# Kernel optimization log

Measured on AMD Instinct MI355X. Metric: run time of the kernel, lower is better.

The kernel has to match this reference:

```python
import jax, jax.numpy as jnp
import numpy as np

HASH_BINS = 100000
EMB = 64
B = 262144


def _glorot(key, shape):
    fan_in, fan_out = shape[0], shape[-1]
    std = np.sqrt(2.0 / (fan_in + fan_out)).astype(np.float32)
    return jax.random.normal(key, shape, dtype=jnp.float32) * std


def setup_inputs() -> dict:
    key = jax.random.key(0)
    ks = jax.random.split(key, 16)
    return {
        "user_idx": jax.random.randint(ks[0], (B,), 0, HASH_BINS, dtype=jnp.int32),
        "item_idx": jax.random.randint(ks[1], (B,), 0, HASH_BINS, dtype=jnp.int32),
        "user_emb": jax.random.normal(ks[2], (HASH_BINS, EMB), dtype=jnp.float32) * 0.05,
        "item_emb": jax.random.normal(ks[3], (HASH_BINS, EMB), dtype=jnp.float32) * 0.05,
        "lin_w": jax.random.normal(ks[4], (2 * HASH_BINS,), dtype=jnp.float32) * 0.01,
        "lin_b": jnp.zeros((1,), jnp.float32),
        "cross_k": _glorot(ks[5], (2 * EMB, 2 * EMB)),
        "W1": _glorot(ks[6], (2 * EMB, 200)), "b1": jnp.zeros((200,), jnp.float32),
        "W2": _glorot(ks[7], (200, 256)),     "b2": jnp.zeros((256,), jnp.float32),
        "W3": _glorot(ks[8], (256, 200)),     "b3": jnp.zeros((200,), jnp.float32),
        "W4": _glorot(ks[9], (200, 128)),     "b4": jnp.zeros((128,), jnp.float32),
        "W5": _glorot(ks[10], (128, 1)),      "b5": jnp.zeros((1,), jnp.float32),
    }


def reference(user_idx, item_idx, user_emb, item_emb, lin_w, lin_b, cross_k,
              W1, b1, W2, b2, W3, b3, W4, b4, W5, b5):
    # Embedding lookups (flattened + concatenated): [B, 2*EMB]
    emb = jnp.concatenate([user_emb[user_idx], item_emb[item_idx]], axis=1)

    # FM linear term. CategoryEncoding(multi-hot over 2*HASH_BINS) -> Dense(1)
    # is exactly a gather-sum of the dense kernel rows (one user + one item token).
    linear = (lin_w[user_idx] + lin_w[HASH_BINS + item_idx] + lin_b)[:, None]  # [B,1]

    # FM cross term: 0.5 * mean((xK)^2 - x^2 K^2, axis=1)
    xk = emb @ cross_k                      # [B, 128]
    x2k2 = (emb * emb) @ (cross_k * cross_k)
    cross = 0.5 * jnp.mean(xk * xk - x2k2, axis=1, keepdims=True)  # [B,1]

    # Deep MLP (inference: no dropout)
    h = jax.nn.relu(emb @ W1 + b1)
    h = jax.nn.relu(h @ W2 + b2)
    h = jax.nn.relu(h @ W3 + b3)
    h = jax.nn.relu(h @ W4 + b4)
    dnn = h @ W5 + b5                       # [B,1]

    return jax.nn.sigmoid(linear + cross + dnn)
```

## Files before the change

### kernel.cpp

```cpp
#include <hip/hip_runtime.h>

#define HASH_BINS 100000
#define EMBD 64
#define BATCH 262144
#define BM 64
#define SA 264
#define SB 232

typedef __attribute__((ext_vector_type(8))) short short8;
typedef __attribute__((ext_vector_type(4))) float floatx4;
typedef __attribute__((ext_vector_type(4))) unsigned short ushortx4;

static __device__ __forceinline__ unsigned short f2bf(float f) {
  unsigned u = __builtin_bit_cast(unsigned, f);
  u += 0x7fff + ((u >> 16) & 1);
  return (unsigned short)(u >> 16);
}
static __device__ __forceinline__ float bf2f(unsigned short b) {
  return __builtin_bit_cast(float, ((unsigned)b) << 16);
}

__global__ void dfm_prep(const float* __restrict__ K, const float* __restrict__ W1,
                         const float* __restrict__ W2, const float* __restrict__ W3,
                         const float* __restrict__ W4,
                         float* __restrict__ S, unsigned short* __restrict__ Kt,
                         unsigned short* __restrict__ W1t, unsigned short* __restrict__ W2t,
                         unsigned short* __restrict__ W3t, unsigned short* __restrict__ W4t)
{
  int idx = blockIdx.x * 256 + threadIdx.x;
  if (idx < 128) {
    float s = 0.f;
    for (int j = 0; j < 128; j++) { float v = K[idx * 128 + j]; s += v * v; }
    S[idx] = s;
  }
  int i = idx;
  if (i < 16384) {
    int k = i >> 7, n = i & 127;
    Kt[n * 128 + k] = f2bf(K[i]);
  } else if ((i -= 16384) < 25600) {
    int k = i / 200, n = i - k * 200;
    W1t[n * 128 + k] = f2bf(W1[i]);
  } else if ((i -= 25600) < 3072) {
    int n = 200 + (i >> 7), k = i & 127;
    W1t[n * 128 + k] = 0;
  } else if ((i -= 3072) < 51200) {
    int k = i >> 8, n = i & 255;
    W2t[n * 224 + k] = f2bf(W2[i]);
  } else if ((i -= 51200) < 6144) {
    int n = i / 24, k = 200 + (i - n * 24);
    W2t[n * 224 + k] = 0;
  } else if ((i -= 6144) < 51200) {
    int k = i / 200, n = i - k * 200;
    W3t[n * 256 + k] = f2bf(W3[i]);
  } else if ((i -= 51200) < 6144) {
    int n = 200 + (i >> 8), k = i & 255;
    W3t[n * 256 + k] = 0;
  } else if ((i -= 6144) < 25600) {
    int k = i >> 7, n = i & 127;
    W4t[n * 224 + k] = f2bf(W4[i]);
  } else if ((i -= 25600) < 3072) {
    int n = i / 24, k = 200 + (i - n * 24);
    W4t[n * 224 + k] = 0;
  }
}

template <int KP, int CH>
static __device__ __forceinline__ void mfma_pass(const unsigned short* __restrict__ wt,
                                                 int tileRow0, const unsigned short* actIn,
                                                 int sin, int m, int qd, floatx4* acc)
{
#pragma unroll
  for (int i = 0; i < CH * 4; i++) acc[i] = {0.f, 0.f, 0.f, 0.f};
#pragma unroll
  for (int ks = 0; ks < KP / 32; ks++) {
    short8 a[4];
#pragma unroll
    for (int rt = 0; rt < 4; rt++)
      a[rt] = *(const short8*)&actIn[(rt * 16 + m) * sin + ks * 32 + qd * 8];
#pragma unroll
    for (int n = 0; n < CH; n++) {
      short8 w = *(const short8*)&wt[(tileRow0 + n * 16 + m) * KP + ks * 32 + qd * 8];
#pragma unroll
      for (int rt = 0; rt < 4; rt++)
        acc[n * 4 + rt] = __builtin_amdgcn_mfma_f32_16x16x32_bf16(w, a[rt], acc[n * 4 + rt], 0, 0, 0);
    }
  }
}

template <int CH>
static __device__ __forceinline__ void epilogue_relu(const float* __restrict__ bias,
                                                     int colBase, int nreal,
                                                     unsigned short* actOut, int sout,
                                                     int m, int qd, const floatx4* acc)
{
#pragma unroll
  for (int n = 0; n < CH; n++) {
    int col = colBase + n * 16 + qd * 4;
    float b0 = 0.f, b1 = 0.f, b2 = 0.f, b3 = 0.f;
    if (col < nreal) {
      float4 q = *(const float4*)(bias + col);
      b0 = q.x; b1 = q.y; b2 = q.z; b3 = q.w;
    }
#pragma unroll
    for (int rt = 0; rt < 4; rt++) {
      ushortx4 h = { f2bf(fmaxf(acc[n * 4 + rt][0] + b0, 0.f)),
                     f2bf(fmaxf(acc[n * 4 + rt][1] + b1, 0.f)),
                     f2bf(fmaxf(acc[n * 4 + rt][2] + b2, 0.f)),
                     f2bf(fmaxf(acc[n * 4 + rt][3] + b3, 0.f)) };
      *(ushortx4*)&actOut[(rt * 16 + m) * sout + col] = h;
    }
  }
}

__global__ __launch_bounds__(512)
void dfm_main(const int* __restrict__ uidx, const int* __restrict__ iidx,
              const float* __restrict__ uemb, const float* __restrict__ iemb,
              const float* __restrict__ linw, const float* __restrict__ linb,
              const float* __restrict__ b1, const float* __restrict__ b2,
              const float* __restrict__ b3, const float* __restrict__ b4,
              const float* __restrict__ W5, const float* __restrict__ b5,
              const float* __restrict__ S, const unsigned short* __restrict__ Wc,
              const unsigned short* __restrict__ W2t, const unsigned short* __restrict__ W3t,
              const unsigned short* __restrict__ W4t,
              float* __restrict__ out)
{
  __shared__ unsigned short actA[BM * SA];
  __shared__ unsigned short actB[BM * SB];
  __shared__ float crosspart[4][BM];
  __shared__ float part[BM][8];
  __shared__ float linrow[BM];

  const int t = threadIdx.x;
  const int lane = t & 63, wave = t >> 6;
  const int m = lane & 15, qd = lane >> 4;
  const int r = t >> 3, c = t & 7;

  {
    int g = blockIdx.x * BM + r;
    int u = uidx[g], it = iidx[g];
    const float* up = uemb + (long)u * EMBD + c * 8;
    const float* ip = iemb + (long)it * EMBD + c * 8;
    float qp = 0.f;
#pragma unroll
    for (int j = 0; j < 8; j += 4) {
      float4 f = *(const float4*)(up + j);
      int col = c * 8 + j;
      float4 sv = *(const float4*)(S + col);
      ushortx4 h = {f2bf(f.x), f2bf(f.y), f2bf(f.z), f2bf(f.w)};
      *(ushortx4*)&actA[r * SA + col] = h;
      qp += f.x * f.x * sv.x + f.y * f.y * sv.y + f.z * f.z * sv.z + f.w * f.w * sv.w;
    }
#pragma unroll
    for (int j = 0; j < 8; j += 4) {
      float4 f = *(const float4*)(ip + j);
      int col = 64 + c * 8 + j;
      float4 sv = *(const float4*)(S + col);
      ushortx4 h = {f2bf(f.x), f2bf(f.y), f2bf(f.z), f2bf(f.w)};
      *(ushortx4*)&actA[r * SA + col] = h;
      qp += f.x * f.x * sv.x + f.y * f.y * sv.y + f.z * f.z * sv.z + f.w * f.w * sv.w;
    }
    part[r][c] = qp;
    if (c == 0) linrow[r] = linw[u] + linw[HASH_BINS + it] + linb[0];
  }
  __syncthreads();

  if (wave < 4) {
    floatx4 acc[8];
    mfma_pass<128, 2>(Wc, (2 * wave) * 16, actA, SA, m, qd, acc);
    float s[4];
#pragma unroll
    for (int rt = 0; rt < 4; rt++) {
      s[rt] = 0.f;
#pragma unroll
      for (int n = 0; n < 2; n++)
#pragma unroll
        for (int i = 0; i < 4; i++)
          s[rt] += acc[n * 4 + rt][i] * acc[n * 4 + rt][i];
      s[rt] += __shfl_xor(s[rt], 16, 64);
      s[rt] += __shfl_xor(s[rt], 32, 64);
    }
    if (qd == 0)
#pragma unroll
      for (int rt = 0; rt < 4; rt++)
        crosspart[wave][rt * 16 + m] = s[rt];
    floatx4 acc2[4];
    mfma_pass<128, 1>(Wc, 128 + wave * 16, actA, SA, m, qd, acc2);
    epilogue_relu<1>(b1, wave * 16, 200, actB, SB, m, qd, acc2);
  } else if (wave < 6) {
    int s0 = 4 + (wave - 4) * 3;
    floatx4 acc[12];
    mfma_pass<128, 3>(Wc, 128 + s0 * 16, actA, SA, m, qd, acc);
    epilogue_relu<3>(b1, s0 * 16, 200, actB, SB, m, qd, acc);
  } else {
    int s0 = 10 + (wave - 6) * 2;
    floatx4 acc[8];
    mfma_pass<128, 2>(Wc, 128 + s0 * 16, actA, SA, m, qd, acc);
    epilogue_relu<2>(b1, s0 * 16, 200, actB, SB, m, qd, acc);
  }
  __syncthreads();

  {
    floatx4 acc[8];
    mfma_pass<224, 2>(W2t, wave * 2 * 16, actB, SB, m, qd, acc);
    epilogue_relu<2>(b2, wave * 2 * 16, 256, actA, SA, m, qd, acc);
  }
  __syncthreads();

  if (wave < 6) {
    floatx4 acc[8];
    mfma_pass<256, 2>(W3t, wave * 2 * 16, actA, SA, m, qd, acc);
    epilogue_relu<2>(b3, wave * 2 * 16, 200, actB, SB, m, qd, acc);
  } else {
    int s0 = 12 + (wave - 6);
    floatx4 acc[4];
    mfma_pass<256, 1>(W3t, s0 * 16, actA, SA, m, qd, acc);
    epilogue_relu<1>(b3, s0 * 16, 200, actB, SB, m, qd, acc);
  }
  __syncthreads();

  {
    floatx4 acc[4];
    mfma_pass<224, 1>(W4t, wave * 16, actB, SB, m, qd, acc);
    epilogue_relu<1>(b4, wave * 16, 128, actA, SA, m, qd, acc);
  }
  __syncthreads();

  {
    float qp = part[r][c];
    float d = 0.f;
    const unsigned short* ap = &actA[r * SA + c * 16];
#pragma unroll
    for (int j = 0; j < 2; j++) {
      short8 h = *(const short8*)(ap + j * 8);
      float4 w0 = *(const float4*)(W5 + c * 16 + j * 8);
      float4 w1 = *(const float4*)(W5 + c * 16 + j * 8 + 4);
      d += bf2f((unsigned short)h[0]) * w0.x + bf2f((unsigned short)h[1]) * w0.y +
           bf2f((unsigned short)h[2]) * w0.z + bf2f((unsigned short)h[3]) * w0.w +
           bf2f((unsigned short)h[4]) * w1.x + bf2f((unsigned short)h[5]) * w1.y +
           bf2f((unsigned short)h[6]) * w1.z + bf2f((unsigned short)h[7]) * w1.w;
    }
    const float inv = 0.5f / 128.f;
    part[r][c] = d - inv * qp;
    __syncthreads();
    if (c == 0) {
      float xk2 = crosspart[0][r] + crosspart[1][r] + crosspart[2][r] + crosspart[3][r];
      float dnn = part[r][0] + part[r][1] + part[r][2] + part[r][3] +
                  part[r][4] + part[r][5] + part[r][6] + part[r][7];
      float logit = linrow[r] + inv * xk2 + dnn + b5[0];
      out[blockIdx.x * BM + r] = 1.f / (1.f + expf(-logit));
    }
  }
}

extern "C" void kernel_launch(void* const* d_in, const int* in_sizes, int n_in,
                              void* d_out, int out_size, void* d_ws, size_t ws_size,
                              hipStream_t stream)
{
  const int*   uidx = (const int*)d_in[0];
  const int*   iidx = (const int*)d_in[1];
  const float* uemb = (const float*)d_in[2];
  const float* iemb = (const float*)d_in[3];
  const float* linw = (const float*)d_in[4];
  const float* linb = (const float*)d_in[5];
  const float* K    = (const float*)d_in[6];
  const float* W1   = (const float*)d_in[7];
  const float* b1   = (const float*)d_in[8];
  const float* W2   = (const float*)d_in[9];
  const float* b2   = (const float*)d_in[10];
  const float* W3   = (const float*)d_in[11];
  const float* b3   = (const float*)d_in[12];
  const float* W4   = (const float*)d_in[13];
  const float* b4   = (const float*)d_in[14];
  const float* W5   = (const float*)d_in[15];
  const float* b5   = (const float*)d_in[16];

  char* w = (char*)d_ws;
  float* S = (float*)w;
  unsigned short* Kt  = (unsigned short*)(w + 512);
  unsigned short* W1t = (unsigned short*)(w + 33280);
  unsigned short* W2t = (unsigned short*)(w + 90624);
  unsigned short* W3t = (unsigned short*)(w + 205312);
  unsigned short* W4t = (unsigned short*)(w + 320000);
  float* out = (float*)d_out;

  dfm_prep<<<736, 256, 0, stream>>>(K, W1, W2, W3, W4, S, Kt, W1t, W2t, W3t, W4t);
  dfm_main<<<BATCH / BM, 512, 0, stream>>>(uidx, iidx, uemb, iemb, linw, linb,
                                           b1, b2, b3, b4, W5, b5,
                                           S, Kt, W2t, W3t, W4t, out);
}
```

Measured before the change: 291.5 us.

## Prefetch first weight fragments before barriers and fuse final layer into MFMA epilogue

Each wave now loads the first K-slice of its weight fragments for the next layer before the preceding __syncthreads, so global/L2 weight latency overlaps the barrier wait. The last hidden layer's ReLU and the W5 dot product are folded into the layer-4 MFMA accumulators with shuffles, which removes the bf16 write-back of layer 4, one barrier and the separate dot-product pass. The prep kernel is rewritten so each thread builds four bf16 values with one vector store, cutting the block count. This costs extra registers for the prefetched fragments and could affect occupancy.

```diff
diff --git a/kernel.cpp b/kernel.cpp
--- a/kernel.cpp
+++ b/kernel.cpp
@@ -27,40 +27,81 @@
                          unsigned short* __restrict__ W1t, unsigned short* __restrict__ W2t,
                          unsigned short* __restrict__ W3t, unsigned short* __restrict__ W4t)
 {
-  int idx = blockIdx.x * 256 + threadIdx.x;
-  if (idx < 128) {
+  int i = blockIdx.x * 256 + threadIdx.x;
+  if (i < 4096) {
+    int n = i >> 5, k4 = (i & 31) * 4;
+    ushortx4 h = { f2bf(K[(k4 + 0) * 128 + n]), f2bf(K[(k4 + 1) * 128 + n]),
+                   f2bf(K[(k4 + 2) * 128 + n]), f2bf(K[(k4 + 3) * 128 + n]) };
+    *(ushortx4*)&Kt[n * 128 + k4] = h;
+  } else if ((i -= 4096) < 7168) {
+    int n = i >> 5, k4 = (i & 31) * 4;
+    ushortx4 h;
+#pragma unroll
+    for (int j = 0; j < 4; j++) h[j] = (n < 200) ? f2bf(W1[(k4 + j) * 200 + n]) : 0;
+    *(ushortx4*)&W1t[n * 128 + k4] = h;
+  } else if ((i -= 7168) < 14336) {
+    int n = i / 56, k4 = (i - n * 56) * 4;
+    ushortx4 h;
+#pragma unroll
+    for (int j = 0; j < 4; j++) h[j] = (k4 + j < 200) ? f2bf(W2[(k4 + j) * 256 + n]) : 0;
+    *(ushortx4*)&W2t[n * 224 + k4] = h;
+  } else if ((i -= 14336) < 14336) {
+    int n = i >> 6, k4 = (i & 63) * 4;
+    ushortx4 h;
+#pragma unroll
+    for (int j = 0; j < 4; j++) h[j] = (n < 200) ? f2bf(W3[(k4 + j) * 200 + n]) : 0;
+    *(ushortx4*)&W3t[n * 256 + k4] = h;
+  } else if ((i -= 14336) < 7168) {
+    int n = i / 56, k4 = (i - n * 56) * 4;
+    ushortx4 h;
+#pragma unroll
+    for (int j = 0; j < 4; j++) h[j] = (k4 + j < 200) ? f2bf(W4[(k4 + j) * 128 + n]) : 0;
+    *(ushortx4*)&W4t[n * 224 + k4] = h;
+  } else if ((i -= 7168) < 128) {
     float s = 0.f;
-    for (int j = 0; j < 128; j++) { float v = K[idx * 128 + j]; s += v * v; }
-    S[idx] = s;
-  }
-  int i = idx;
-  if (i < 16384) {
-    int k = i >> 7, n = i & 127;
-    Kt[n * 128 + k] = f2bf(K[i]);
-  } else if ((i -= 16384) < 25600) {
-    int k = i / 200, n = i - k * 200;
-    W1t[n * 128 + k] = f2bf(W1[i]);
-  } else if ((i -= 25600) < 3072) {
-    int n = 200 + (i >> 7), k = i & 127;
-    W1t[n * 128 + k] = 0;
-  } else if ((i -= 3072) < 51200) {
-    int k = i >> 8, n = i & 255;
-    W2t[n * 224 + k] = f2bf(W2[i]);
-  } else if ((i -= 51200) < 6144) {
-    int n = i / 24, k = 200 + (i - n * 24);
-    W2t[n * 224 + k] = 0;
-  } else if ((i -= 6144) < 51200) {
-    int k = i / 200, n = i - k * 200;
-    W3t[n * 256 + k] = f2bf(W3[i]);
-  } else if ((i -= 51200) < 6144) {
-    int n = 200 + (i >> 8), k = i & 255;
-    W3t[n * 256 + k] = 0;
-  } else if ((i -= 6144) < 25600) {
-    int k = i >> 7, n = i & 127;
-    W4t[n * 224 + k] = f2bf(W4[i]);
-  } else if ((i -= 25600) < 3072) {
-    int n = i / 24, k = 200 + (i - n * 24);
-    W4t[n * 224 + k] = 0;
+    for (int j = 0; j < 128; j++) { float v = K[i * 128 + j]; s += v * v; }
+    S[i] = s;
+  }
+}
+
+template <int KP, int CH>
+static __device__ __forceinline__ void wpref(const unsigned short* __restrict__ wt,
+                                             int tileRow0, int m, int qd, short8* wpre)
+{
+#pragma unroll
+  for (int n = 0; n < CH; n++)
+    wpre[n] = *(const short8*)&wt[(tileRow0 + n * 16 + m) * KP + qd * 8];
+}
+
+template <int KP, int CH>
+static __device__ __forceinline__ void mfma_pass_pre(const unsigned short* __restrict__ wt,
+                                                     int tileRow0, const unsigned short* actIn,
+                                                     int sin, int m, int qd, floatx4* acc,
+                                                     const short8* wpre)
+{
+#pragma unroll
+  for (int i = 0; i < CH * 4; i++) acc[i] = {0.f, 0.f, 0.f, 0.f};
+  short8 a[4];
+#pragma unroll
+  for (int rt = 0; rt < 4; rt++)
+    a[rt] = *(const short8*)&actIn[(rt * 16 + m) * sin + qd * 8];
+#pragma unroll
+  for (int n = 0; n < CH; n++)
+#pragma unroll
+    for (int rt = 0; rt < 4; rt++)
+      acc[n * 4 + rt] = __builtin_amdgcn_mfma_f32_16x16x32_bf16(wpre[n], a[rt], acc[n * 4 + rt], 0, 0, 0);
+#pragma unroll
+  for (int ks = 1; ks < KP / 32; ks++) {
+#pragma unroll
+    for (int rt = 0; rt < 4; rt++)
+      a[rt] = *(const short8*)&actIn[(rt * 16 + m) * sin + ks * 32 + qd * 8];
+#pragma unroll
+    for (int n = 0; n < CH; n++) {
+      short8 w = *(const short8*)&wt[(tileRow0 + n * 16 + m) * KP + ks * 32 + qd * 8];
+#pragma unroll
+      for (int rt = 0; rt < 4; rt++)
+        acc[n * 4 + rt] = __builtin_amdgcn_mfma_f32_16x16x32_bf16(w, a[rt], acc[n * 4 + rt], 0, 0, 0);
+    }
   }
 }
 
@@ -128,6 +169,7 @@
   __shared__ unsigned short actB[BM * SB];
   __shared__ float crosspart[4][BM];
   __shared__ float part[BM][8];
+  __shared__ float qpart[BM][8];
   __shared__ float linrow[BM];
 
   const int t = threadIdx.x;
@@ -159,14 +201,19 @@
       *(ushortx4*)&actA[r * SA + col] = h;
       qp += f.x * f.x * sv.x + f.y * f.y * sv.y + f.z * f.z * sv.z + f.w * f.w * sv.w;
     }
-    part[r][c] = qp;
+    qpart[r][c] = qp;
     if (c == 0) linrow[r] = linw[u] + linw[HASH_BINS + it] + linb[0];
   }
+
+  short8 wpre[3];
+  if (wave < 4)      wpref<128, 2>(Wc, 2 * wave * 16, m, qd, wpre);
+  else if (wave < 6) wpref<128, 3>(Wc, 128 + (4 + (wave - 4) * 3) * 16, m, qd, wpre);
+  else               wpref<128, 2>(Wc, 128 + (10 + (wave - 6) * 2) * 16, m, qd, wpre);
   __syncthreads();
 
   if (wave < 4) {
     floatx4 acc[8];
-    mfma_pass<128, 2>(Wc, (2 * wave) * 16, actA, SA, m, qd, acc);
+    mfma_pass_pre<128, 2>(Wc, 2 * wave * 16, actA, SA, m, qd, acc, wpre);
     float s[4];
 #pragma unroll
     for (int rt = 0; rt < 4; rt++) {
@@ -189,66 +236,68 @@
   } else if (wave < 6) {
     int s0 = 4 + (wave - 4) * 3;
     floatx4 acc[12];
-    mfma_pass<128, 3>(Wc, 128 + s0 * 16, actA, SA, m, qd, acc);
+    mfma_pass_pre<128, 3>(Wc, 128 + s0 * 16, actA, SA, m, qd, acc, wpre);
     epilogue_relu<3>(b1, s0 * 16, 200, actB, SB, m, qd, acc);
   } else {
     int s0 = 10 + (wave - 6) * 2;
     floatx4 acc[8];
-    mfma_pass<128, 2>(Wc, 128 + s0 * 16, actA, SA, m, qd, acc);
+    mfma_pass_pre<128, 2>(Wc, 128 + s0 * 16, actA, SA, m, qd, acc, wpre);
     epilogue_relu<2>(b1, s0 * 16, 200, actB, SB, m, qd, acc);
   }
+  wpref<224, 2>(W2t, wave * 32, m, qd, wpre);
   __syncthreads();
 
   {
     floatx4 acc[8];
-    mfma_pass<224, 2>(W2t, wave * 2 * 16, actB, SB, m, qd, acc);
-    epilogue_relu<2>(b2, wave * 2 * 16, 256, actA, SA, m, qd, acc);
-  }
+    mfma_pass_pre<224, 2>(W2t, wave * 32, actB, SB, m, qd, acc, wpre);
+    epilogue_relu<2>(b2, wave * 32, 256, actA, SA, m, qd, acc);
+  }
+  if (wave < 6) wpref<256, 2>(W3t, wave * 32, m, qd, wpre);
+  else          wpref<256, 1>(W3t, (12 + (wave - 6)) * 16, m, qd, wpre);
   __syncthreads();
 
   if (wave < 6) {
     floatx4 acc[8];
-    mfma_pass<256, 2>(W3t, wave * 2 * 16, actA, SA, m, qd, acc);
-    epilogue_relu<2>(b3, wave * 2 * 16, 200, actB, SB, m, qd, acc);
+    mfma_pass_pre<256, 2>(W3t, wave * 32, actA, SA, m, qd, acc, wpre);
+    epilogue_relu<2>(b3, wave * 32, 200, actB, SB, m, qd, acc);
   } else {
-    int s0 = 12 + (wave - 6);
+    int s0 = (12 + (wave - 6)) * 16;
     floatx4 acc[4];
-    mfma_pass<256, 1>(W3t, s0 * 16, actA, SA, m, qd, acc);
-    epilogue_relu<1>(b3, s0 * 16, 200, actB, SB, m, qd, acc);
-  }
+    mfma_pass_pre<256, 1>(W3t, s0, actA, SA, m, qd, acc, wpre);
+    epilogue_relu<1>(b3, s0, 200, actB, SB, m, qd, acc);
+  }
+  wpref<224, 1>(W4t, wave * 16, m, qd, wpre);
   __syncthreads();
 
   {
     floatx4 acc[4];
-    mfma_pass<224, 1>(W4t, wave * 16, actB, SB, m, qd, acc);
-    epilogue_relu<1>(b4, wave * 16, 128, actA, SA, m, qd, acc);
-  }
-  __syncthreads();
-
-  {
-    float qp = part[r][c];
-    float d = 0.f;
-    const unsigned short* ap = &actA[r * SA + c * 16];
-#pragma unroll
-    for (int j = 0; j < 2; j++) {
-      short8 h = *(const short8*)(ap + j * 8);
-      float4 w0 = *(const float4*)(W5 + c * 16 + j * 8);
-      float4 w1 = *(const float4*)(W5 + c * 16 + j * 8 + 4);
-      d += bf2f((unsigned short)h[0]) * w0.x + bf2f((unsigned short)h[1]) * w0.y +
-           bf2f((unsigned short)h[2]) * w0.z + bf2f((unsigned short)h[3]) * w0.w +
-           bf2f((unsigned short)h[4]) * w1.x + bf2f((unsigned short)h[5]) * w1.y +
-           bf2f((unsigned short)h[6]) * w1.z + bf2f((unsigned short)h[7]) * w1.w;
-    }
+    mfma_pass_pre<224, 1>(W4t, wave * 16, actB, SB, m, qd, acc, wpre);
+    int nb = wave * 16 + qd * 4;
+    float4 w5q = *(const float4*)(W5 + nb);
+    float4 b4q = *(const float4*)(b4 + nb);
+#pragma unroll
+    for (int rt = 0; rt < 4; rt++) {
+      float s = fmaxf(acc[rt][0] + b4q.x, 0.f) * w5q.x +
+                fmaxf(acc[rt][1] + b4q.y, 0.f) * w5q.y +
+                fmaxf(acc[rt][2] + b4q.z, 0.f) * w5q.z +
+                fmaxf(acc[rt][3] + b4q.w, 0.f) * w5q.w;
+      s += __shfl_xor(s, 16, 64);
+      s += __shfl_xor(s, 32, 64);
+      if (qd == 0) part[rt * 16 + m][wave] = s;
+    }
+  }
+  __syncthreads();
+
+  if (t < BM) {
+    int rr = t;
+    float xk2 = crosspart[0][rr] + crosspart[1][rr] + crosspart[2][rr] + crosspart[3][rr];
+    float qs = qpart[rr][0] + qpart[rr][1] + qpart[rr][2] + qpart[rr][3] +
+               qpart[rr][4] + qpart[rr][5] + qpart[rr][6] + qpart[rr][7];
+    float dnn = part[rr][0] + part[rr][1] + part[rr][2] + part[rr][3] +
+                part[rr][4] + part[rr][5] + part[rr][6] + part[rr][7];
     const float inv = 0.5f / 128.f;
-    part[r][c] = d - inv * qp;
-    __syncthreads();
-    if (c == 0) {
-      float xk2 = crosspart[0][r] + crosspart[1][r] + crosspart[2][r] + crosspart[3][r];
-      float dnn = part[r][0] + part[r][1] + part[r][2] + part[r][3] +
-                  part[r][4] + part[r][5] + part[r][6] + part[r][7];
-      float logit = linrow[r] + inv * xk2 + dnn + b5[0];
-      out[blockIdx.x * BM + r] = 1.f / (1.f + expf(-logit));
-    }
+    float logit = linrow[rr] + inv * (xk2 - qs) + dnn + b5[0];
+    out[blockIdx.x * BM + rr] = 1.f / (1.f + expf(-logit));
   }
 }
 
@@ -283,7 +332,7 @@
   unsigned short* W4t = (unsigned short*)(w + 320000);
   float* out = (float*)d_out;
 
-  dfm_prep<<<736, 256, 0, stream>>>(K, W1, W2, W3, W4, S, Kt, W1t, W2t, W3t, W4t);
+  dfm_prep<<<185, 256, 0, stream>>>(K, W1, W2, W3, W4, S, Kt, W1t, W2t, W3t, W4t);
   dfm_main<<<BATCH / BM, 512, 0, stream>>>(uidx, iidx, uemb, iemb, linw, linb,
                                            b1, b2, b3, b4, W5, b5,
                                            S, Kt, W2t, W3t, W4t, out);
```

After: 278.4 us. 4.5% less time.
